# Optimization experiments

Measured on AMD Instinct MI355X. Metric: run time of the kernel, lower is better.

## Reference

```python
import jax, jax.numpy as jnp
import numpy as np

B, C, H, W = 8, 512, 64, 64
CI = 256  # inter_channels = channel_in // 2
EPS = 1e-5  # BatchNorm eps


def conv1x1(x, w, b):
    # x: (b, c, h, w), w: (o, c), b: (o,)
    return jnp.einsum('bchw,oc->bohw', x, w) + b[None, :, None, None]


def maxpool2(x):
    b, c, h, w = x.shape
    return x.reshape(b, c, h // 2, 2, w // 2, 2).max(axis=(3, 5))


def setup_inputs() -> dict:
    key = jax.random.key(0)
    ks = jax.random.split(key, 13)
    s = 1.0 / np.sqrt(C)
    si = 1.0 / np.sqrt(CI)
    return {
        'x': jax.random.normal(ks[0], (B, C, H, W), dtype=jnp.float32),
        'w_g': jax.random.normal(ks[1], (CI, C), dtype=jnp.float32) * s,
        'b_g': jax.random.normal(ks[2], (CI,), dtype=jnp.float32) * 0.01,
        'w_theta': jax.random.normal(ks[3], (CI, C), dtype=jnp.float32) * s,
        'b_theta': jax.random.normal(ks[4], (CI,), dtype=jnp.float32) * 0.01,
        'w_phi': jax.random.normal(ks[5], (CI, C), dtype=jnp.float32) * s,
        'b_phi': jax.random.normal(ks[6], (CI,), dtype=jnp.float32) * 0.01,
        'w_out': jax.random.normal(ks[7], (C, CI), dtype=jnp.float32) * si,
        'b_out': jax.random.normal(ks[8], (C,), dtype=jnp.float32) * 0.01,
        'bn_gamma': jax.random.normal(ks[9], (C,), dtype=jnp.float32) * 0.1 + 1.0,
        'bn_beta': jax.random.normal(ks[10], (C,), dtype=jnp.float32) * 0.01,
        'bn_mean': jax.random.normal(ks[11], (C,), dtype=jnp.float32) * 0.01,
        'bn_var': jax.random.uniform(ks[12], (C,), dtype=jnp.float32, minval=0.5, maxval=1.5),
    }


def reference(x, w_g, b_g, w_theta, b_theta, w_phi, b_phi,
              w_out, b_out, bn_gamma, bn_beta, bn_mean, bn_var):
    b = x.shape[0]
    # g, phi: 1x1 conv then 2x2 maxpool (sub_sample=True)
    g_x = maxpool2(conv1x1(x, w_g, b_g)).reshape(b, CI, -1)        # (b, ci, M)
    phi_x = maxpool2(conv1x1(x, w_phi, b_phi)).reshape(b, CI, -1)  # (b, ci, M)
    theta_x = conv1x1(x, w_theta, b_theta).reshape(b, CI, -1)      # (b, ci, N)
    # f[b, n, m] = theta^T @ phi  -> softmax over m -> @ g^T
    f = jnp.einsum('bcn,bcm->bnm', theta_x, phi_x)                 # (b, N, M)
    attn = jax.nn.softmax(f, axis=-1)
    y = jnp.einsum('bnm,bcm->bcn', attn, g_x).reshape(b, CI, H, W)
    # W: 1x1 conv + BatchNorm (eval mode, running stats)
    w_y = conv1x1(y, w_out, b_out)
    inv = bn_gamma / jnp.sqrt(bn_var + EPS)
    w_y = w_y * inv[None, :, None, None] + (bn_beta - bn_mean * inv)[None, :, None, None]
    return w_y + x
```

## Files before the change

kernel.cpp:

```cpp
#include <hip/hip_runtime.h>

typedef _Float16 v8h __attribute__((ext_vector_type(8)));
typedef _Float16 v4h __attribute__((ext_vector_type(4)));
typedef float v4f __attribute__((ext_vector_type(4)));
#define HF _Float16

#define Bn 8
#define Cc 512
#define CI 256
#define HW 4096
#define Mp 1024

__device__ __forceinline__ void gload16(const void* g, void* l) {
    __builtin_amdgcn_global_load_lds((const __attribute__((address_space(1))) void*)g,
                                     (__attribute__((address_space(3))) void*)l, 16, 0, 0);
}

__global__ __launch_bounds__(256) void prep_kernel(
    const float* __restrict__ w_g, const float* __restrict__ b_g,
    const float* __restrict__ w_th, const float* __restrict__ b_th,
    const float* __restrict__ w_ph, const float* __restrict__ b_ph,
    const float* __restrict__ w_out, const float* __restrict__ b_out,
    const float* __restrict__ gamma, const float* __restrict__ beta,
    const float* __restrict__ mean, const float* __restrict__ var,
    HF* __restrict__ wall, float* __restrict__ ball,
    HF* __restrict__ wo, float* __restrict__ scale, float* __restrict__ shift)
{
    int idx = blockIdx.x * 256 + threadIdx.x;
    if (idx < 768*512) {
        int o = idx >> 9;
        float v = (o < 256) ? w_th[idx] : (o < 512) ? w_ph[idx - 256*512] : w_g[idx - 512*512];
        wall[idx] = (HF)v;
    }
    if (idx < 512*256) wo[idx] = (HF)w_out[idx];
    if (idx < 768) ball[idx] = (idx < 256) ? b_th[idx] : (idx < 512) ? b_ph[idx-256] : b_g[idx-512];
    if (idx < 512) {
        float inv = gamma[idx] * rsqrtf(var[idx] + 1e-5f);
        scale[idx] = inv;
        shift[idx] = (b_out[idx] - mean[idx]) * inv + beta[idx];
    }
}

__global__ __launch_bounds__(256) void transpose_x_kernel(const float* __restrict__ x, HF* __restrict__ xT)
{
    __shared__ float tile[64][65];
    int b = blockIdx.z;
    int c0 = blockIdx.y * 64, s0 = blockIdx.x * 64;
    int tr = threadIdx.x >> 6, ts = threadIdx.x & 63;
    #pragma unroll
    for (int i = 0; i < 16; ++i) {
        int r = tr + i*4;
        tile[r][ts] = x[((long)(b*Cc) + c0 + r)*HW + s0 + ts];
    }
    __syncthreads();
    #pragma unroll
    for (int i = 0; i < 16; ++i) {
        int r = tr + i*4;
        xT[((long)b*HW + s0 + r)*Cc + c0 + ts] = (HF)tile[ts][r];
    }
}

__global__ __launch_bounds__(256) void pool_sm_kernel(const HF* __restrict__ TP, HF* __restrict__ Pt)
{
    int idx = blockIdx.x * 256 + threadIdx.x;
    int c8 = idx & 31;
    int m  = (idx >> 5) & 1023;
    int b  = idx >> 15;
    int h2 = m >> 5, w2 = m & 31;
    int s00 = h2*128 + w2*2;
    const HF* base = TP + ((long)b*HW + s00)*512 + 256 + c8*8;
    v8h a0 = *(const v8h*)(base);
    v8h a1 = *(const v8h*)(base + 512);
    v8h a2 = *(const v8h*)(base + 64*512);
    v8h a3 = *(const v8h*)(base + 65*512);
    v8h o;
    #pragma unroll
    for (int j = 0; j < 8; ++j) {
        float v = fmaxf(fmaxf((float)a0[j], (float)a1[j]), fmaxf((float)a2[j], (float)a3[j]));
        o[j] = (HF)v;
    }
    *(v8h*)(Pt + ((long)b*Mp + m)*CI + c8*8) = o;
}

__global__ __launch_bounds__(256) void pool_kernel(const HF* __restrict__ src, long sSrc,
                                                   HF* __restrict__ dst, long sDst)
{
    long idx = (long)blockIdx.x * 256 + threadIdx.x;
    int m = idx & 1023;
    long bc = idx >> 10;
    int c = (int)(bc & 255);
    int b = (int)(bc >> 8);
    int h2 = m >> 5, w2 = m & 31;
    const HF* p = src + (long)b*sSrc + (long)c*HW + h2*128 + w2*2;
    float v = fmaxf(fmaxf((float)p[0], (float)p[1]), fmaxf((float)p[64], (float)p[65]));
    dst[(long)b*sDst + (long)c*Mp + m] = (HF)v;
}

template<int EPI>
__global__ __launch_bounds__(256) void gemm_bt_kernel(
    const HF* __restrict__ A, long sA, const HF* __restrict__ B, long sB,
    void* __restrict__ Cv, long sC, int M, int N, int K,
    const float* __restrict__ bias,
    const float* __restrict__ rowScale, const float* __restrict__ rowShift,
    const float* __restrict__ Xres, long sX)
{
    __shared__ HF As[128][40];
    __shared__ HF Bs[128][40];
    int b = blockIdx.z;
    int i0 = blockIdx.y * 128;
    int j0 = blockIdx.x * 128;
    const HF* Ab = A + (long)b * sA;
    const HF* Bb = B + (long)b * sB;
    int tid = threadIdx.x;
    int lane = tid & 63, w = tid >> 6;
    int wr = w >> 1, wc = w & 1;
    int lr = lane & 15, lk = (lane >> 4) * 8;

    v4f acc[4][4];
    #pragma unroll
    for (int i = 0; i < 4; ++i)
        #pragma unroll
        for (int j = 0; j < 4; ++j) { v4f z = {0.f,0.f,0.f,0.f}; acc[i][j] = z; }

    for (int k0 = 0; k0 < K; k0 += 32) {
        #pragma unroll
        for (int q = 0; q < 2; ++q) {
            int ch = tid*2 + q;
            int row = ch >> 2;
            int c8 = (ch & 3) * 8;
            const uint4* ga = (const uint4*)(Ab + (long)(i0+row)*K + k0 + c8);
            *(uint4*)(&As[row][c8]) = *ga;
            const uint4* gb = (const uint4*)(Bb + (long)(j0+row)*K + k0 + c8);
            *(uint4*)(&Bs[row][c8]) = *gb;
        }
        __syncthreads();
        v8h af[4], bfr[4];
        #pragma unroll
        for (int mf = 0; mf < 4; ++mf)
            af[mf] = *(const v8h*)(&As[wr*64 + mf*16 + lr][lk]);
        #pragma unroll
        for (int nf = 0; nf < 4; ++nf)
            bfr[nf] = *(const v8h*)(&Bs[wc*64 + nf*16 + lr][lk]);
        #pragma unroll
        for (int mf = 0; mf < 4; ++mf)
            #pragma unroll
            for (int nf = 0; nf < 4; ++nf)
                acc[mf][nf] = __builtin_amdgcn_mfma_f32_16x16x32_f16(af[mf], bfr[nf], acc[mf][nf], 0, 0, 0);
        __syncthreads();
    }

    int rbase = (lane >> 4) * 4;
    #pragma unroll
    for (int mf = 0; mf < 4; ++mf) {
        #pragma unroll
        for (int nf = 0; nf < 4; ++nf) {
            #pragma unroll
            for (int r = 0; r < 4; ++r) {
                int row = i0 + wr*64 + mf*16 + rbase + r;
                int col = j0 + wc*64 + nf*16 + lr;
                float v = acc[mf][nf][r];
                if (EPI == 0) {
                    v += bias[row];
                    ((HF*)Cv + (long)b*sC)[(long)row*N + col] = (HF)v;
                } else if (EPI == 3) {
                    v += bias[col];
                    ((HF*)Cv + (long)b*sC)[(long)row*N + col] = (HF)v;
                } else {
                    float* Cf = (float*)Cv + (long)b*sC;
                    const float* Xb = Xres + (long)b*sX;
                    long o = (long)row*N + col;
                    Cf[o] = v * rowScale[row] + rowShift[row] + Xb[o];
                }
            }
        }
    }
}

__global__ __launch_bounds__(256, 2) void fused_attn_kernel(
    const HF* __restrict__ TP,
    const HF* __restrict__ Pt,
    const HF* __restrict__ G,
    HF* __restrict__ Yt)
{
    __shared__ alignas(16) HF P_lds[2][8192];
    __shared__ alignas(16) HF P_buf[2][4][16][36];
    __shared__ float smem_a[2][4][16];
    __shared__ float smem_l[64];

    int bid = blockIdx.x;
    int b = bid & 7;
    int ntile = bid >> 3;
    int tid = threadIdx.x;
    int lane = tid & 63, w = tid >> 6;
    int lr = lane & 15, lkg = lane >> 4;
    int nbase = ntile * 64;

    const HF* Tq = TP + ((long)b*HW + nbase + w*16) * 512;
    const HF* Pb = Pt + (long)b*Mp*CI;
    const HF* Gb = G  + (long)b*CI*Mp + (long)(w*64)*Mp;

    auto stage = [&](int bsel, int m0) {
        #pragma unroll
        for (int q = 0; q < 4; ++q) {
            int idxp = (w*4 + q)*64 + lane;
            int pkg = idxp >> 5, prow = idxp & 31;
            gload16(Pb + (long)(m0 + prow)*CI + pkg*8, P_lds[bsel] + (size_t)idxp*8);
        }
    };
    auto loadG = [&](int m0, v8h* g) {
        #pragma unroll
        for (int ct = 0; ct < 4; ++ct)
            g[ct] = *(const v8h*)(Gb + (long)(ct*16 + lr)*Mp + m0 + lkg*8);
    };

    v8h af[8];
    #pragma unroll
    for (int kf = 0; kf < 8; ++kf)
        af[kf] = *(const v8h*)(Tq + (long)lr*512 + kf*32 + lkg*8);

    v4f acc_y[4][4];
    #pragma unroll
    for (int i = 0; i < 4; ++i)
        #pragma unroll
        for (int j = 0; j < 4; ++j) { v4f z = {0.f,0.f,0.f,0.f}; acc_y[i][j] = z; }
    float mrun[4] = {-1e30f,-1e30f,-1e30f,-1e30f};
    float lsum[4] = {0.f,0.f,0.f,0.f};

    v8h gA[4], gB[4];
    stage(0, 0);
    loadG(0, gA);
    __syncthreads();

    #pragma unroll 2
    for (int t = 0; t < 32; ++t) {
        int cur = t & 1;
        int pb = t & 1;
        v8h* gcur  = (t & 1) ? gB : gA;
        v8h* gnext = (t & 1) ? gA : gB;
        if (t < 31) {
            stage(cur ^ 1, (t+1)*32);
            loadG((t+1)*32, gnext);
        }

        v4f acc[2];
        #pragma unroll
        for (int nf = 0; nf < 2; ++nf) { v4f z = {0.f,0.f,0.f,0.f}; acc[nf] = z; }
        __builtin_amdgcn_s_setprio(1);
        #pragma unroll
        for (int kf = 0; kf < 8; ++kf) {
            #pragma unroll
            for (int nf = 0; nf < 2; ++nf) {
                v8h bfr = *(const v8h*)(P_lds[cur] + (kf*4 + lkg)*256 + (nf*16 + lr)*8);
                acc[nf] = __builtin_amdgcn_mfma_f32_16x16x32_f16(af[kf], bfr, acc[nf], 0, 0, 0);
            }
        }
        __builtin_amdgcn_s_setprio(0);

        #pragma unroll
        for (int r = 0; r < 4; ++r) {
            float cm = fmaxf(acc[0][r], acc[1][r]);
            #pragma unroll
            for (int d = 1; d < 16; d <<= 1) cm = fmaxf(cm, __shfl_xor(cm, d));
            float alpha = 1.f;
            if (cm > mrun[r]) {
                alpha = __expf(mrun[r] - cm);
                mrun[r] = cm;
                lsum[r] *= alpha;
            }
            int row = lkg*4 + r;
            if (lr == 0) smem_a[pb][w][row] = alpha;
            #pragma unroll
            for (int nf = 0; nf < 2; ++nf) {
                float p = __expf(acc[nf][r] - mrun[r]);
                lsum[r] += p;
                P_buf[pb][w][row][nf*16 + lr] = (HF)p;
            }
        }

        __syncthreads();

        __builtin_amdgcn_s_setprio(1);
        #pragma unroll
        for (int rt = 0; rt < 4; ++rt) {
            v8h ap;
            {
                v4h a0 = *(const v4h*)(&P_buf[pb][rt][lr][lkg*8]);
                v4h a1 = *(const v4h*)(&P_buf[pb][rt][lr][lkg*8 + 4]);
                ap = __builtin_shufflevector(a0, a1, 0,1,2,3,4,5,6,7);
            }
            float al0 = smem_a[pb][rt][lkg*4 + 0];
            float al1 = smem_a[pb][rt][lkg*4 + 1];
            float al2 = smem_a[pb][rt][lkg*4 + 2];
            float al3 = smem_a[pb][rt][lkg*4 + 3];
            #pragma unroll
            for (int ct = 0; ct < 4; ++ct) {
                acc_y[rt][ct][0] *= al0;
                acc_y[rt][ct][1] *= al1;
                acc_y[rt][ct][2] *= al2;
                acc_y[rt][ct][3] *= al3;
                acc_y[rt][ct] = __builtin_amdgcn_mfma_f32_16x16x32_f16(ap, gcur[ct], acc_y[rt][ct], 0, 0, 0);
            }
        }
        __builtin_amdgcn_s_setprio(0);
    }

    #pragma unroll
    for (int r = 0; r < 4; ++r) {
        float s = lsum[r];
        #pragma unroll
        for (int d = 1; d < 16; d <<= 1) s += __shfl_xor(s, d);
        if (lr == 0) smem_l[w*16 + lkg*4 + r] = s;
    }
    __syncthreads();
    HF* Yb = Yt + ((long)b*HW + nbase) * CI;
    #pragma unroll
    for (int rt = 0; rt < 4; ++rt) {
        #pragma unroll
        for (int r = 0; r < 4; ++r) {
            int row = rt*16 + lkg*4 + r;
            float inv = 1.f / smem_l[row];
            #pragma unroll
            for (int ct = 0; ct < 4; ++ct)
                Yb[(long)row*CI + w*64 + ct*16 + lr] = (HF)(acc_y[rt][ct][r] * inv);
        }
    }
}

extern "C" void kernel_launch(void* const* d_in, const int* in_sizes, int n_in,
                              void* d_out, int out_size, void* d_ws, size_t ws_size,
                              hipStream_t stream)
{
    const float* x     = (const float*)d_in[0];
    const float* w_g   = (const float*)d_in[1];
    const float* b_g   = (const float*)d_in[2];
    const float* w_th  = (const float*)d_in[3];
    const float* b_th  = (const float*)d_in[4];
    const float* w_ph  = (const float*)d_in[5];
    const float* b_ph  = (const float*)d_in[6];
    const float* w_out = (const float*)d_in[7];
    const float* b_out = (const float*)d_in[8];
    const float* gamma = (const float*)d_in[9];
    const float* beta  = (const float*)d_in[10];
    const float* mean  = (const float*)d_in[11];
    const float* var   = (const float*)d_in[12];
    float* out = (float*)d_out;

    char* ws = (char*)d_ws;
    size_t off = 0;
    auto alloc = [&](size_t bytes) { void* p = ws + off; off += (bytes + 255) & ~(size_t)255; return p; };
    HF*    wall  = (HF*)alloc((size_t)768*512*2);
    float* ball  = (float*)alloc(768*4);
    HF*    wo    = (HF*)alloc((size_t)512*256*2);
    float* scale = (float*)alloc(512*4);
    float* shift = (float*)alloc(512*4);
    HF*    xT    = (HF*)alloc((size_t)Bn*HW*Cc*2);
    HF*    TP    = (HF*)alloc((size_t)Bn*HW*512*2);
    HF*    Gg    = (HF*)alloc((size_t)Bn*CI*HW*2);
    HF*    Pt    = (HF*)alloc((size_t)Bn*Mp*CI*2);
    HF*    G     = (HF*)alloc((size_t)Bn*CI*Mp*2);
    HF*    Yt    = (HF*)alloc((size_t)Bn*HW*CI*2);

    prep_kernel<<<1536, 256, 0, stream>>>(w_g,b_g,w_th,b_th,w_ph,b_ph,w_out,b_out,gamma,beta,mean,var,
                                          wall, ball, wo, scale, shift);
    transpose_x_kernel<<<dim3(64,8,Bn), 256, 0, stream>>>(x, xT);
    gemm_bt_kernel<3><<<dim3(4,32,Bn), 256, 0, stream>>>(xT, (long)HW*Cc, wall, 0, TP, (long)HW*512,
                                                         HW, 512, Cc, ball, nullptr, nullptr, nullptr, 0);
    gemm_bt_kernel<0><<<dim3(32,2,Bn), 256, 0, stream>>>(wall + (size_t)512*512, 0, xT, (long)HW*Cc,
                                                         Gg, (long)CI*HW, CI, HW, Cc, ball + 512,
                                                         nullptr, nullptr, nullptr, 0);
    pool_sm_kernel<<<1024, 256, 0, stream>>>(TP, Pt);
    pool_kernel<<<8192, 256, 0, stream>>>(Gg, (long)CI*HW, G, (long)CI*Mp);
    fused_attn_kernel<<<512, 256, 0, stream>>>(TP, Pt, G, Yt);
    gemm_bt_kernel<2><<<dim3(32,4,Bn), 256, 0, stream>>>(wo, 0, Yt, (long)HW*CI, out, (long)Cc*HW,
                                                         Cc, HW, CI, nullptr, scale, shift, x, (long)Cc*HW);
}
```

Baseline: 206.0 us.

## Transpose QK MFMA so each lane owns a row and skip rescale lazily

Swaps the MFMA operands in the score computation so each lane holds scores for a single query row. Row max and sum then need only two cross-lane shuffles instead of four per register. It adds a lazy online-softmax rescale that only updates the running max when it grows by more than 7, and skips the accumulator rescale when no alpha differs from one. This cuts shuffle and VALU work in the softmax, at the cost of a slightly larger exponent range in fp16 probabilities and the removal of the unroll-2 pragma.

```diff
diff --git a/kernel.cpp b/kernel.cpp
--- a/kernel.cpp
+++ b/kernel.cpp
@@ -184,7 +184,7 @@
 {
     __shared__ alignas(16) HF P_lds[2][8192];
     __shared__ alignas(16) HF P_buf[2][4][16][36];
-    __shared__ float smem_a[2][4][16];
+    __shared__ alignas(16) float smem_a[2][4][16];
     __shared__ float smem_l[64];
 
     int bid = blockIdx.x;
@@ -223,15 +223,14 @@
     for (int i = 0; i < 4; ++i)
         #pragma unroll
         for (int j = 0; j < 4; ++j) { v4f z = {0.f,0.f,0.f,0.f}; acc_y[i][j] = z; }
-    float mrun[4] = {-1e30f,-1e30f,-1e30f,-1e30f};
-    float lsum[4] = {0.f,0.f,0.f,0.f};
+    float mrun = -1e30f;
+    float lsum = 0.f;
 
     v8h gA[4], gB[4];
     stage(0, 0);
     loadG(0, gA);
     __syncthreads();
 
-    #pragma unroll 2
     for (int t = 0; t < 32; ++t) {
         int cur = t & 1;
         int pb = t & 1;
@@ -244,42 +243,61 @@
 
         v4f acc[2];
         #pragma unroll
-        for (int nf = 0; nf < 2; ++nf) { v4f z = {0.f,0.f,0.f,0.f}; acc[nf] = z; }
+        for (int mt = 0; mt < 2; ++mt) { v4f z = {0.f,0.f,0.f,0.f}; acc[mt] = z; }
         __builtin_amdgcn_s_setprio(1);
         #pragma unroll
         for (int kf = 0; kf < 8; ++kf) {
             #pragma unroll
-            for (int nf = 0; nf < 2; ++nf) {
-                v8h bfr = *(const v8h*)(P_lds[cur] + (kf*4 + lkg)*256 + (nf*16 + lr)*8);
-                acc[nf] = __builtin_amdgcn_mfma_f32_16x16x32_f16(af[kf], bfr, acc[nf], 0, 0, 0);
+            for (int mt = 0; mt < 2; ++mt) {
+                v8h pf = *(const v8h*)(P_lds[cur] + (kf*4 + lkg)*256 + (mt*16 + lr)*8);
+                acc[mt] = __builtin_amdgcn_mfma_f32_16x16x32_f16(pf, af[kf], acc[mt], 0, 0, 0);
             }
         }
         __builtin_amdgcn_s_setprio(0);
 
-        #pragma unroll
-        for (int r = 0; r < 4; ++r) {
-            float cm = fmaxf(acc[0][r], acc[1][r]);
-            #pragma unroll
-            for (int d = 1; d < 16; d <<= 1) cm = fmaxf(cm, __shfl_xor(cm, d));
-            float alpha = 1.f;
-            if (cm > mrun[r]) {
-                alpha = __expf(mrun[r] - cm);
-                mrun[r] = cm;
-                lsum[r] *= alpha;
+        float cm = fmaxf(fmaxf(fmaxf(acc[0][0], acc[0][1]), fmaxf(acc[0][2], acc[0][3])),
+                         fmaxf(fmaxf(acc[1][0], acc[1][1]), fmaxf(acc[1][2], acc[1][3])));
+        cm = fmaxf(cm, __shfl_xor(cm, 16));
+        cm = fmaxf(cm, __shfl_xor(cm, 32));
+        float alpha = 1.f;
+        if (cm > mrun + 7.f) {
+            alpha = __expf(mrun - cm);
+            mrun = cm;
+            lsum *= alpha;
+        }
+        if (lane < 16) smem_a[pb][w][lr] = alpha;
+        #pragma unroll
+        for (int mt = 0; mt < 2; ++mt) {
+            v4h p4;
+            #pragma unroll
+            for (int r = 0; r < 4; ++r) {
+                float p = __expf(acc[mt][r] - mrun);
+                lsum += p;
+                p4[r] = (HF)p;
             }
-            int row = lkg*4 + r;
-            if (lr == 0) smem_a[pb][w][row] = alpha;
-            #pragma unroll
-            for (int nf = 0; nf < 2; ++nf) {
-                float p = __expf(acc[nf][r] - mrun[r]);
-                lsum[r] += p;
-                P_buf[pb][w][row][nf*16 + lr] = (HF)p;
-            }
+            *(v4h*)(&P_buf[pb][w][lr][mt*16 + lkg*4]) = p4;
         }
 
         __syncthreads();
 
         __builtin_amdgcn_s_setprio(1);
+        v4f alv[4];
+        bool need = false;
+        #pragma unroll
+        for (int rt = 0; rt < 4; ++rt) {
+            alv[rt] = *(const v4f*)(&smem_a[pb][rt][lkg*4]);
+            need = need | (alv[rt][0] != 1.f) | (alv[rt][1] != 1.f)
+                        | (alv[rt][2] != 1.f) | (alv[rt][3] != 1.f);
+        }
+        if (__any(need)) {
+            #pragma unroll
+            for (int rt = 0; rt < 4; ++rt)
+                #pragma unroll
+                for (int ct = 0; ct < 4; ++ct)
+                    #pragma unroll
+                    for (int r = 0; r < 4; ++r)
+                        acc_y[rt][ct][r] *= alv[rt][r];
+        }
         #pragma unroll
         for (int rt = 0; rt < 4; ++rt) {
             v8h ap;
@@ -288,29 +306,16 @@
                 v4h a1 = *(const v4h*)(&P_buf[pb][rt][lr][lkg*8 + 4]);
                 ap = __builtin_shufflevector(a0, a1, 0,1,2,3,4,5,6,7);
             }
-            float al0 = smem_a[pb][rt][lkg*4 + 0];
-            float al1 = smem_a[pb][rt][lkg*4 + 1];
-            float al2 = smem_a[pb][rt][lkg*4 + 2];
-            float al3 = smem_a[pb][rt][lkg*4 + 3];
-            #pragma unroll
-            for (int ct = 0; ct < 4; ++ct) {
-                acc_y[rt][ct][0] *= al0;
-                acc_y[rt][ct][1] *= al1;
-                acc_y[rt][ct][2] *= al2;
-                acc_y[rt][ct][3] *= al3;
+            #pragma unroll
+            for (int ct = 0; ct < 4; ++ct)
                 acc_y[rt][ct] = __builtin_amdgcn_mfma_f32_16x16x32_f16(ap, gcur[ct], acc_y[rt][ct], 0, 0, 0);
-            }
         }
         __builtin_amdgcn_s_setprio(0);
     }
 
-    #pragma unroll
-    for (int r = 0; r < 4; ++r) {
-        float s = lsum[r];
-        #pragma unroll
-        for (int d = 1; d < 16; d <<= 1) s += __shfl_xor(s, d);
-        if (lr == 0) smem_l[w*16 + lkg*4 + r] = s;
-    }
+    lsum += __shfl_xor(lsum, 16);
+    lsum += __shfl_xor(lsum, 32);
+    if (lane < 16) smem_l[w*16 + lr] = lsum;
     __syncthreads();
     HF* Yb = Yt + ((long)b*HW + nbase) * CI;
     #pragma unroll
```

Result: faster. 201.1 us (-2.4%).
